# Optimization experiments

Hardware: AMD Instinct MI355X
Metric: run time of the kernel (lower is better)

The kernel has to match this reference:

```python
import jax, jax.numpy as jnp
import numpy as np

B, D, C = 1024, 128, 100000
EPS = 1e-12  # torch F.normalize eps


def setup_inputs() -> dict:
    key = jax.random.key(0)
    k1, k2, k3 = jax.random.split(key, 3)
    # scale so ||x||^2 ~ 1, keeping exp(-dist) in a representable range
    xs = jax.random.normal(k1, (B, D), dtype=jnp.float32) / np.sqrt(D)
    ys = jax.random.randint(k2, (B,), 0, C, dtype=jnp.int64)
    # xavier_uniform init of Embedding(C, D): U(-a, a), a = sqrt(6/(C+D))
    a = np.sqrt(6.0 / (C + D))
    proxies = jax.random.uniform(k3, (C, D), dtype=jnp.float32, minval=-a, maxval=a)
    return {"xs": xs, "ys": ys, "proxies": proxies}


def reference(xs, ys, proxies):
    # L2-normalize every proxy (original normalizes pos proxy over dim=0 of a 1-D
    # vector and neg proxies over dim=1 -- both are per-proxy L2 normalization).
    norm = jnp.linalg.norm(proxies, axis=1, keepdims=True)
    P = proxies / jnp.maximum(norm, EPS)                      # [C, D], unit rows
    x_sq = jnp.sum(xs * xs, axis=1, keepdims=True)            # [B, 1]
    d = x_sq + 1.0 - 2.0 * (xs @ P.T)                         # [B, C]
    e = jnp.exp(-d)                                           # [B, C]
    pos = jnp.take_along_axis(e, ys[:, None], axis=1)[:, 0]   # exp(-d[b, y_b])
    neg_sum = jnp.sum(e, axis=1) - pos                        # denominator excludes the positive
    return jnp.mean(-jnp.log(pos / neg_sum))
```

## Files before the change

kernel.cpp:

```cpp
#include <hip/hip_runtime.h>
#include <hip/hip_fp16.h>

#define B_N 1024
#define D_K 128
#define C_N 100000
#define CT_PER_CHUNK 5
#define CCHUNK (CT_PER_CHUNK * 32)
#define NCHUNK (C_N / CCHUNK)
#define BSPLIT 2
#define NBLK_MAIN (NCHUNK * BSPLIT)
#define NREP 64
#define NPROXY_BLK (C_N / 32)
#define EPSN 1e-12f

typedef _Float16 half8 __attribute__((ext_vector_type(8)));
typedef float floatx16 __attribute__((ext_vector_type(16)));

union U16 { uint4 u; half8 h; };

__device__ __forceinline__ unsigned int pack2h(float a, float b) {
    union { _Float16 h[2]; unsigned int u; } p;
    p.h[0] = (_Float16)a; p.h[1] = (_Float16)b;
    return p.u;
}

__global__ __launch_bounds__(256) void prep_kernel(
    const float* __restrict__ xs, const int* __restrict__ ys,
    const float* __restrict__ proxies,
    uint4* __restrict__ pfrag, unsigned int* __restrict__ xfrag,
    float* __restrict__ w, float* __restrict__ posd,
    float* __restrict__ negsumR)
{
    int tid = threadIdx.x, bx = blockIdx.x;

    if (bx < NPROXY_BLK) {
        int L = tid & 7;
        int r = tid >> 3;
        int c = bx * 32 + r;
        const float4* src = (const float4*)(proxies + (size_t)c * D_K + L * 16);
        float4 v0 = src[0], v1 = src[1], v2 = src[2], v3 = src[3];
        float ss = v0.x*v0.x + v0.y*v0.y + v0.z*v0.z + v0.w*v0.w
                 + v1.x*v1.x + v1.y*v1.y + v1.z*v1.z + v1.w*v1.w
                 + v2.x*v2.x + v2.y*v2.y + v2.z*v2.z + v2.w*v2.w
                 + v3.x*v3.x + v3.y*v3.y + v3.z*v3.z + v3.w*v3.w;
        ss += __shfl_xor(ss, 1, 64);
        ss += __shfl_xor(ss, 2, 64);
        ss += __shfl_xor(ss, 4, 64);
        float sc = 1.0f / fmaxf(sqrtf(ss), EPSN);

        union { _Float16 h[8]; uint4 u; } pa, pb;
        pa.h[0]=(_Float16)(v0.x*sc); pa.h[1]=(_Float16)(v0.y*sc);
        pa.h[2]=(_Float16)(v0.z*sc); pa.h[3]=(_Float16)(v0.w*sc);
        pa.h[4]=(_Float16)(v1.x*sc); pa.h[5]=(_Float16)(v1.y*sc);
        pa.h[6]=(_Float16)(v1.z*sc); pa.h[7]=(_Float16)(v1.w*sc);
        pb.h[0]=(_Float16)(v2.x*sc); pb.h[1]=(_Float16)(v2.y*sc);
        pb.h[2]=(_Float16)(v2.z*sc); pb.h[3]=(_Float16)(v2.w*sc);
        pb.h[4]=(_Float16)(v3.x*sc); pb.h[5]=(_Float16)(v3.y*sc);
        pb.h[6]=(_Float16)(v3.z*sc); pb.h[7]=(_Float16)(v3.w*sc);

        uint4* dst = pfrag + (size_t)bx * 512;
        dst[L * 64 + r]      = pa.u;
        dst[L * 64 + 32 + r] = pb.u;
    } else {
        int bb = bx - NPROXY_BLK;
        negsumR[bb * 256 + tid] = 0.0f;

        int wave = tid >> 6, lane = tid & 63;
        int b = bb * 4 + wave;
        const float2 xv = ((const float2*)(xs + (size_t)b * D_K))[lane];
        float ss = xv.x * xv.x + xv.y * xv.y;
        #pragma unroll
        for (int m = 1; m < 64; m <<= 1) ss += __shfl_xor(ss, m, 64);
        float xsq = ss;

        int ks = lane >> 3, kh = (lane >> 2) & 1, jq = lane & 3;
        int idx = (((b >> 5) * 8 + ks) * 64 + ((b & 31) | (kh << 5))) * 4 + jq;
        xfrag[idx] = pack2h(2.0f * xv.x, 2.0f * xv.y);

        int y = ys[b];
        const float2 pv = ((const float2*)(proxies + (size_t)y * D_K))[lane];
        float dt = xv.x * pv.x + xv.y * pv.y;
        float pp = pv.x * pv.x + pv.y * pv.y;
        #pragma unroll
        for (int m = 1; m < 64; m <<= 1) {
            dt += __shfl_xor(dt, m, 64);
            pp += __shfl_xor(pp, m, 64);
        }
        if (lane == 0) {
            w[b] = __expf(-xsq - 1.0f);
            float nrm = fmaxf(sqrtf(pp), EPSN);
            posd[b] = xsq + 1.0f - 2.0f * (dt / nrm);
        }
    }
}

__device__ __forceinline__ void compute_pair(
    const uint4* ldsP, int lane,
    const uint4 xfA[8], const uint4 xfB[8],
    float& outA, float& outB)
{
    float sA0 = 0.f, sA1 = 0.f, sB0 = 0.f, sB1 = 0.f;
    #pragma unroll 1
    for (int ct = 0; ct < CT_PER_CHUNK; ++ct) {
        uint4 a[8];
        #pragma unroll
        for (int k = 0; k < 8; ++k)
            a[k] = ldsP[(ct * 8 + k) * 64 + lane];

        floatx16 accA, accB;
        #pragma unroll
        for (int i = 0; i < 16; ++i) { accA[i] = 0.0f; accB[i] = 0.0f; }

        #pragma unroll
        for (int k = 0; k < 8; ++k) {
            U16 ua, u0, u1;
            ua.u = a[k]; u0.u = xfA[k]; u1.u = xfB[k];
            accA = __builtin_amdgcn_mfma_f32_32x32x16_f16(ua.h, u0.h, accA, 0, 0, 0);
            accB = __builtin_amdgcn_mfma_f32_32x32x16_f16(ua.h, u1.h, accB, 0, 0, 0);
        }

        #pragma unroll
        for (int i = 0; i < 16; i += 2) {
            sA0 += __expf(accA[i]);     sA1 += __expf(accA[i + 1]);
            sB0 += __expf(accB[i]);     sB1 += __expf(accB[i + 1]);
        }
    }
    outA = sA0 + sA1;
    outB = sB0 + sB1;
}

__global__ __launch_bounds__(256, 3) void main_kernel(
    const uint4* __restrict__ pfrag, const uint4* __restrict__ xfrag,
    const float* __restrict__ w, float* __restrict__ negsumR)
{
    __shared__ uint4 ldsP[CT_PER_CHUNK * 8 * 64];

    int tid = threadIdx.x, wave = tid >> 6, lane = tid & 63;
    int bx = blockIdx.x;
    int cchunk = bx >> 1;
    int bs = bx & 1;

    {
        const uint4* src = pfrag + (size_t)cchunk * (CT_PER_CHUNK * 8 * 64);
        #pragma unroll
        for (int i = 0; i < 10; ++i) {
            int f = wave * 10 + i;
            __builtin_amdgcn_global_load_lds(
                (const __attribute__((address_space(1))) void*)(src + f * 64 + lane),
                (__attribute__((address_space(3))) void*)(ldsP + f * 64),
                16, 0, 0);
        }
    }

    int nt0 = bs * 16 + wave * 4;
    uint4 xfA[8], xfB[8];
    #pragma unroll
    for (int k = 0; k < 8; ++k) xfA[k] = xfrag[((nt0    ) * 8 + k) * 64 + lane];
    #pragma unroll
    for (int k = 0; k < 8; ++k) xfB[k] = xfrag[((nt0 + 1) * 8 + k) * 64 + lane];

    __syncthreads();

    int rep = bx & (NREP - 1);
    float* nsr = negsumR + (size_t)rep * B_N;

    float s0, s1;
    compute_pair(ldsP, lane, xfA, xfB, s0, s1);

    #pragma unroll
    for (int k = 0; k < 8; ++k) xfA[k] = xfrag[((nt0 + 2) * 8 + k) * 64 + lane];
    #pragma unroll
    for (int k = 0; k < 8; ++k) xfB[k] = xfrag[((nt0 + 3) * 8 + k) * 64 + lane];

    s0 += __shfl_xor(s0, 32, 64);
    s1 += __shfl_xor(s1, 32, 64);
    if (lane < 32) {
        int b0 = (nt0    ) * 32 + lane;
        int b1 = (nt0 + 1) * 32 + lane;
        atomicAdd(&nsr[b0], s0 * w[b0]);
        atomicAdd(&nsr[b1], s1 * w[b1]);
    }

    float s2, s3;
    compute_pair(ldsP, lane, xfA, xfB, s2, s3);
    s2 += __shfl_xor(s2, 32, 64);
    s3 += __shfl_xor(s3, 32, 64);
    if (lane < 32) {
        int b2 = (nt0 + 2) * 32 + lane;
        int b3 = (nt0 + 3) * 32 + lane;
        atomicAdd(&nsr[b2], s2 * w[b2]);
        atomicAdd(&nsr[b3], s3 * w[b3]);
    }
}

__global__ __launch_bounds__(1024) void final_kernel(
    const float* __restrict__ negsumR, const float* __restrict__ posd,
    float* __restrict__ out)
{
    __shared__ float red[1024];
    int t = threadIdx.x;
    float ns = 0.0f;
    #pragma unroll 4
    for (int r = 0; r < NREP; ++r) ns += negsumR[r * B_N + t];
    float pd = posd[t];
    red[t] = logf(ns - __expf(-pd)) + pd;
    __syncthreads();
    #pragma unroll
    for (int s = 512; s > 0; s >>= 1) {
        if (t < s) red[t] += red[t + s];
        __syncthreads();
    }
    if (t == 0) out[0] = red[0] * (1.0f / 1024.0f);
}

extern "C" void kernel_launch(void* const* d_in, const int* in_sizes, int n_in,
                              void* d_out, int out_size, void* d_ws, size_t ws_size,
                              hipStream_t stream)
{
    const float* xs      = (const float*)d_in[0];
    const int*   ys      = (const int*)d_in[1];
    const float* proxies = (const float*)d_in[2];

    char* ws = (char*)d_ws;
    uint4*        pfrag   = (uint4*)ws;
    unsigned int* xfrag   = (unsigned int*)(ws + 25600000);
    float*        w       = (float*)(ws + 25600000 + 262144);
    float*        posd    = (float*)(ws + 25600000 + 262144 + 4096);
    float*        negsumR = (float*)(ws + 25600000 + 262144 + 8192);

    prep_kernel<<<NPROXY_BLK + 256, 256, 0, stream>>>(
        xs, ys, proxies, pfrag, xfrag, w, posd, negsumR);
    main_kernel<<<NBLK_MAIN, 256, 0, stream>>>(
        pfrag, (const uint4*)xfrag, w, negsumR);
    final_kernel<<<1, 1024, 0, stream>>>(negsumR, posd, (float*)d_out);
}
```

Baseline: 130.8 us.

## Fuse proxy normalization into main kernel and use exp2 with prescaled x

Proxy L2 normalization and fp16 packing now happen inside the main kernel, written straight to LDS, so the intermediate fp16 proxy buffer is no longer written to and read back from global memory. The x fragments are prescaled by 2*log2(e), which lets the inner loop use the hardware exp2 instead of __expf. The catch is that each proxy chunk is now read and normalized twice, once per batch split, and the normalization work sits in the main kernel's prologue instead of being overlapped or amortized.

```diff
diff --git a/kernel.cpp b/kernel.cpp
--- a/kernel.cpp
+++ b/kernel.cpp
@@ -10,13 +10,15 @@
 #define BSPLIT 2
 #define NBLK_MAIN (NCHUNK * BSPLIT)
 #define NREP 64
-#define NPROXY_BLK (C_N / 32)
+#define K2LOG2E 2.8853900817779268f
 #define EPSN 1e-12f
 
 typedef _Float16 half8 __attribute__((ext_vector_type(8)));
 typedef float floatx16 __attribute__((ext_vector_type(16)));
 
 union U16 { uint4 u; half8 h; };
+
+#define EXP2F(x) __builtin_amdgcn_exp2f(x)
 
 __device__ __forceinline__ unsigned int pack2h(float a, float b) {
     union { _Float16 h[2]; unsigned int u; } p;
@@ -27,70 +29,37 @@
 __global__ __launch_bounds__(256) void prep_kernel(
     const float* __restrict__ xs, const int* __restrict__ ys,
     const float* __restrict__ proxies,
-    uint4* __restrict__ pfrag, unsigned int* __restrict__ xfrag,
-    float* __restrict__ w, float* __restrict__ posd,
-    float* __restrict__ negsumR)
-{
-    int tid = threadIdx.x, bx = blockIdx.x;
-
-    if (bx < NPROXY_BLK) {
-        int L = tid & 7;
-        int r = tid >> 3;
-        int c = bx * 32 + r;
-        const float4* src = (const float4*)(proxies + (size_t)c * D_K + L * 16);
-        float4 v0 = src[0], v1 = src[1], v2 = src[2], v3 = src[3];
-        float ss = v0.x*v0.x + v0.y*v0.y + v0.z*v0.z + v0.w*v0.w
-                 + v1.x*v1.x + v1.y*v1.y + v1.z*v1.z + v1.w*v1.w
-                 + v2.x*v2.x + v2.y*v2.y + v2.z*v2.z + v2.w*v2.w
-                 + v3.x*v3.x + v3.y*v3.y + v3.z*v3.z + v3.w*v3.w;
-        ss += __shfl_xor(ss, 1, 64);
-        ss += __shfl_xor(ss, 2, 64);
-        ss += __shfl_xor(ss, 4, 64);
-        float sc = 1.0f / fmaxf(sqrtf(ss), EPSN);
-
-        union { _Float16 h[8]; uint4 u; } pa, pb;
-        pa.h[0]=(_Float16)(v0.x*sc); pa.h[1]=(_Float16)(v0.y*sc);
-        pa.h[2]=(_Float16)(v0.z*sc); pa.h[3]=(_Float16)(v0.w*sc);
-        pa.h[4]=(_Float16)(v1.x*sc); pa.h[5]=(_Float16)(v1.y*sc);
-        pa.h[6]=(_Float16)(v1.z*sc); pa.h[7]=(_Float16)(v1.w*sc);
-        pb.h[0]=(_Float16)(v2.x*sc); pb.h[1]=(_Float16)(v2.y*sc);
-        pb.h[2]=(_Float16)(v2.z*sc); pb.h[3]=(_Float16)(v2.w*sc);
-        pb.h[4]=(_Float16)(v3.x*sc); pb.h[5]=(_Float16)(v3.y*sc);
-        pb.h[6]=(_Float16)(v3.z*sc); pb.h[7]=(_Float16)(v3.w*sc);
-
-        uint4* dst = pfrag + (size_t)bx * 512;
-        dst[L * 64 + r]      = pa.u;
-        dst[L * 64 + 32 + r] = pb.u;
-    } else {
-        int bb = bx - NPROXY_BLK;
-        negsumR[bb * 256 + tid] = 0.0f;
-
-        int wave = tid >> 6, lane = tid & 63;
-        int b = bb * 4 + wave;
-        const float2 xv = ((const float2*)(xs + (size_t)b * D_K))[lane];
-        float ss = xv.x * xv.x + xv.y * xv.y;
-        #pragma unroll
-        for (int m = 1; m < 64; m <<= 1) ss += __shfl_xor(ss, m, 64);
-        float xsq = ss;
-
-        int ks = lane >> 3, kh = (lane >> 2) & 1, jq = lane & 3;
-        int idx = (((b >> 5) * 8 + ks) * 64 + ((b & 31) | (kh << 5))) * 4 + jq;
-        xfrag[idx] = pack2h(2.0f * xv.x, 2.0f * xv.y);
-
-        int y = ys[b];
-        const float2 pv = ((const float2*)(proxies + (size_t)y * D_K))[lane];
-        float dt = xv.x * pv.x + xv.y * pv.y;
-        float pp = pv.x * pv.x + pv.y * pv.y;
-        #pragma unroll
-        for (int m = 1; m < 64; m <<= 1) {
-            dt += __shfl_xor(dt, m, 64);
-            pp += __shfl_xor(pp, m, 64);
-        }
-        if (lane == 0) {
-            w[b] = __expf(-xsq - 1.0f);
-            float nrm = fmaxf(sqrtf(pp), EPSN);
-            posd[b] = xsq + 1.0f - 2.0f * (dt / nrm);
-        }
+    unsigned int* __restrict__ xfrag, float* __restrict__ w,
+    float* __restrict__ posd, float* __restrict__ negsumR)
+{
+    int tid = threadIdx.x, bb = blockIdx.x;
+    negsumR[bb * 256 + tid] = 0.0f;
+
+    int wave = tid >> 6, lane = tid & 63;
+    int b = bb * 4 + wave;
+    const float2 xv = ((const float2*)(xs + (size_t)b * D_K))[lane];
+    float ss = xv.x * xv.x + xv.y * xv.y;
+    #pragma unroll
+    for (int m = 1; m < 64; m <<= 1) ss += __shfl_xor(ss, m, 64);
+    float xsq = ss;
+
+    int ks = lane >> 3, kh = (lane >> 2) & 1, jq = lane & 3;
+    int idx = (((b >> 5) * 8 + ks) * 64 + ((b & 31) | (kh << 5))) * 4 + jq;
+    xfrag[idx] = pack2h(K2LOG2E * xv.x, K2LOG2E * xv.y);
+
+    int y = ys[b];
+    const float2 pv = ((const float2*)(proxies + (size_t)y * D_K))[lane];
+    float dt = xv.x * pv.x + xv.y * pv.y;
+    float pp = pv.x * pv.x + pv.y * pv.y;
+    #pragma unroll
+    for (int m = 1; m < 64; m <<= 1) {
+        dt += __shfl_xor(dt, m, 64);
+        pp += __shfl_xor(pp, m, 64);
+    }
+    if (lane == 0) {
+        w[b] = __expf(-xsq - 1.0f);
+        float nrm = fmaxf(sqrtf(pp), EPSN);
+        posd[b] = xsq + 1.0f - 2.0f * (dt / nrm);
     }
 }
 
@@ -121,8 +90,8 @@
 
         #pragma unroll
         for (int i = 0; i < 16; i += 2) {
-            sA0 += __expf(accA[i]);     sA1 += __expf(accA[i + 1]);
-            sB0 += __expf(accB[i]);     sB1 += __expf(accB[i + 1]);
+            sA0 += EXP2F(accA[i]);     sA1 += EXP2F(accA[i + 1]);
+            sB0 += EXP2F(accB[i]);     sB1 += EXP2F(accB[i + 1]);
         }
     }
     outA = sA0 + sA1;
@@ -130,25 +99,46 @@
 }
 
 __global__ __launch_bounds__(256, 3) void main_kernel(
-    const uint4* __restrict__ pfrag, const uint4* __restrict__ xfrag,
+    const float* __restrict__ proxies,
+    const uint4* __restrict__ xfrag,
     const float* __restrict__ w, float* __restrict__ negsumR)
 {
     __shared__ uint4 ldsP[CT_PER_CHUNK * 8 * 64];
 
     int tid = threadIdx.x, wave = tid >> 6, lane = tid & 63;
     int bx = blockIdx.x;
-    int cchunk = bx >> 1;
+    int c0 = (bx >> 1) * CCHUNK;
     int bs = bx & 1;
 
     {
-        const uint4* src = pfrag + (size_t)cchunk * (CT_PER_CHUNK * 8 * 64);
-        #pragma unroll
-        for (int i = 0; i < 10; ++i) {
-            int f = wave * 10 + i;
-            __builtin_amdgcn_global_load_lds(
-                (const __attribute__((address_space(1))) void*)(src + f * 64 + lane),
-                (__attribute__((address_space(3))) void*)(ldsP + f * 64),
-                16, 0, 0);
+        int L = tid & 7;
+        int r = tid >> 3;
+        #pragma unroll 1
+        for (int p = 0; p < CT_PER_CHUNK; ++p) {
+            int c = c0 + p * 32 + r;
+            const float4* src = (const float4*)(proxies + (size_t)c * D_K + L * 16);
+            float4 v0 = src[0], v1 = src[1], v2 = src[2], v3 = src[3];
+            float ss = v0.x*v0.x + v0.y*v0.y + v0.z*v0.z + v0.w*v0.w
+                     + v1.x*v1.x + v1.y*v1.y + v1.z*v1.z + v1.w*v1.w
+                     + v2.x*v2.x + v2.y*v2.y + v2.z*v2.z + v2.w*v2.w
+                     + v3.x*v3.x + v3.y*v3.y + v3.z*v3.z + v3.w*v3.w;
+            ss += __shfl_xor(ss, 1, 64);
+            ss += __shfl_xor(ss, 2, 64);
+            ss += __shfl_xor(ss, 4, 64);
+            float sc = 1.0f / fmaxf(sqrtf(ss), EPSN);
+
+            union { _Float16 h[8]; uint4 u; } pa, pb;
+            pa.h[0]=(_Float16)(v0.x*sc); pa.h[1]=(_Float16)(v0.y*sc);
+            pa.h[2]=(_Float16)(v0.z*sc); pa.h[3]=(_Float16)(v0.w*sc);
+            pa.h[4]=(_Float16)(v1.x*sc); pa.h[5]=(_Float16)(v1.y*sc);
+            pa.h[6]=(_Float16)(v1.z*sc); pa.h[7]=(_Float16)(v1.w*sc);
+            pb.h[0]=(_Float16)(v2.x*sc); pb.h[1]=(_Float16)(v2.y*sc);
+            pb.h[2]=(_Float16)(v2.z*sc); pb.h[3]=(_Float16)(v2.w*sc);
+            pb.h[4]=(_Float16)(v3.x*sc); pb.h[5]=(_Float16)(v3.y*sc);
+            pb.h[6]=(_Float16)(v3.z*sc); pb.h[7]=(_Float16)(v3.w*sc);
+
+            ldsP[p * 512 + L * 64 + r]      = pa.u;
+            ldsP[p * 512 + L * 64 + 32 + r] = pb.u;
         }
     }
 
@@ -222,15 +212,12 @@
     const float* proxies = (const float*)d_in[2];
 
     char* ws = (char*)d_ws;
-    uint4*        pfrag   = (uint4*)ws;
-    unsigned int* xfrag   = (unsigned int*)(ws + 25600000);
-    float*        w       = (float*)(ws + 25600000 + 262144);
-    float*        posd    = (float*)(ws + 25600000 + 262144 + 4096);
-    float*        negsumR = (float*)(ws + 25600000 + 262144 + 8192);
-
-    prep_kernel<<<NPROXY_BLK + 256, 256, 0, stream>>>(
-        xs, ys, proxies, pfrag, xfrag, w, posd, negsumR);
-    main_kernel<<<NBLK_MAIN, 256, 0, stream>>>(
-        pfrag, (const uint4*)xfrag, w, negsumR);
+    unsigned int* xfrag   = (unsigned int*)ws;
+    float*        w       = (float*)(ws + 262144);
+    float*        posd    = (float*)(ws + 262144 + 4096);
+    float*        negsumR = (float*)(ws + 262144 + 8192);
+
+    prep_kernel<<<256, 256, 0, stream>>>(xs, ys, proxies, xfrag, w, posd, negsumR);
+    main_kernel<<<NBLK_MAIN, 256, 0, stream>>>(proxies, (const uint4*)xfrag, w, negsumR);
     final_kernel<<<1, 1024, 0, stream>>>(negsumR, posd, (float*)d_out);
 }
```

Result: faster. 125.3 us (-4.2%).
